# Kernel optimization log

Hardware: AMD Instinct MI355X
Metric: run time of the kernel (lower is better)

## Reference

```python
import jax, jax.numpy as jnp
import numpy as np

TEMP = 0.1
GROUPS = 16
EPS = 1e-5
COS_EPS = 1e-8


def _encoder(x, conv_w, conv_b, gn_g, gn_b):
    # Conv2d(C,C,3,pad=1) -> GroupNorm(16,C) -> ReLU -> AdaptiveAvgPool2d(1) -> Flatten
    y = jax.lax.conv_general_dilated(
        x, conv_w, window_strides=(1, 1), padding='SAME',
        dimension_numbers=('NCHW', 'OIHW', 'NCHW')) + conv_b[None, :, None, None]
    B, C, H, W = y.shape
    yg = y.reshape(B, GROUPS, C // GROUPS, H, W)
    mu = yg.mean(axis=(2, 3, 4), keepdims=True)
    var = yg.var(axis=(2, 3, 4), keepdims=True)
    yn = ((yg - mu) * jax.lax.rsqrt(var + EPS)).reshape(B, C, H, W)
    y = yn * gn_g[None, :, None, None] + gn_b[None, :, None, None]
    y = jax.nn.relu(y)
    return y.mean(axis=(2, 3))  # [B, C]


def _projector(h, w1, b1, w2, b2, ln_g, ln_b):
    h = jax.nn.relu(h @ w1 + b1)
    h = h @ w2 + b2
    mu = h.mean(axis=-1, keepdims=True)
    var = h.var(axis=-1, keepdims=True)
    return (h - mu) * jax.lax.rsqrt(var + EPS) * ln_g + ln_b


def _predictor(z, w1, b1, w2, b2):
    return jax.nn.relu(z @ w1 + b1) @ w2 + b2


def _l2norm(z):
    n = jnp.sqrt(jnp.sum(z * z, axis=1, keepdims=True))
    return z / jnp.maximum(n, COS_EPS)


def _pair_loss(zi, zj, off_idx):
    # vectorized version of the nested-loop cosine-sim + cross-entropy (label 0)
    S = (_l2norm(zi) @ _l2norm(zj).T) / TEMP  # [B, B]
    pos = jnp.diagonal(S)                     # sim(i_k, j_k)
    neg = jnp.take_along_axis(S, off_idx, axis=1)  # [B, B-1], row k = S[k, l!=k]
    logits = jnp.concatenate([pos[:, None], neg], axis=1)
    return jnp.mean(jax.nn.logsumexp(logits, axis=1) - logits[:, 0])


def setup_inputs() -> dict:
    key = jax.random.key(0)
    ks = jax.random.split(key, 32)
    B, C, H, W, P = 256, 256, 16, 16, 128
    d = {}
    d['x_t2w'] = jax.random.normal(ks[0], (B, C, H, W), jnp.float32)
    d['x_t2f'] = jax.random.normal(ks[1], (B, C, H, W), jnp.float32)
    d['x_t1n'] = jax.random.normal(ks[2], (B, C, H, W), jnp.float32)
    i = 3
    for m in ('t2w', 't2f', 't1n'):
        d[f'conv_w_{m}'] = jax.random.normal(ks[i], (C, C, 3, 3), jnp.float32) * 0.02; i += 1
        d[f'conv_b_{m}'] = jnp.zeros((C,), jnp.float32)
        d[f'gn_g_{m}'] = jnp.ones((C,), jnp.float32)
        d[f'gn_b_{m}'] = jnp.zeros((C,), jnp.float32)
    d['proj_w1'] = jax.random.normal(ks[i], (C, C), jnp.float32) * 0.02; i += 1
    d['proj_b1'] = jnp.zeros((C,), jnp.float32)
    d['proj_w2'] = jax.random.normal(ks[i], (C, P), jnp.float32) * 0.02; i += 1
    d['proj_b2'] = jnp.zeros((P,), jnp.float32)
    d['ln_g'] = jnp.ones((P,), jnp.float32)
    d['ln_b'] = jnp.zeros((P,), jnp.float32)
    d['pred_w1'] = jax.random.normal(ks[i], (P, P), jnp.float32) * 0.02; i += 1
    d['pred_b1'] = jnp.zeros((P,), jnp.float32)
    d['pred_w2'] = jax.random.normal(ks[i], (P, P), jnp.float32) * 0.02; i += 1
    d['pred_b2'] = jnp.zeros((P,), jnp.float32)
    return d


def reference(x_t2w, x_t2f, x_t1n,
              conv_w_t2w, conv_b_t2w, gn_g_t2w, gn_b_t2w,
              conv_w_t2f, conv_b_t2f, gn_g_t2f, gn_b_t2f,
              conv_w_t1n, conv_b_t1n, gn_g_t1n, gn_b_t1n,
              proj_w1, proj_b1, proj_w2, proj_b2, ln_g, ln_b,
              pred_w1, pred_b1, pred_w2, pred_b2):
    xs = [x_t2w, x_t2f, x_t1n]
    enc_params = [(conv_w_t2w, conv_b_t2w, gn_g_t2w, gn_b_t2w),
                  (conv_w_t2f, conv_b_t2f, gn_g_t2f, gn_b_t2f),
                  (conv_w_t1n, conv_b_t1n, gn_g_t1n, gn_b_t1n)]
    encoded = [_encoder(x, *p) for x, p in zip(xs, enc_params)]
    projected = [_projector(e, proj_w1, proj_b1, proj_w2, proj_b2, ln_g, ln_b) for e in encoded]
    preds = [_predictor(z, pred_w1, pred_b1, pred_w2, pred_b2) for z in projected]

    B = projected[0].shape[0]
    off_idx = jnp.asarray(np.array([[l for l in range(B) if l != k] for k in range(B)],
                                    dtype=np.int32))
    pairs = [(0, 1), (0, 2), (1, 2)]
    loss = sum(_pair_loss(projected[i], projected[j], off_idx) for i, j in pairs) / len(pairs)

    return (jnp.stack(encoded), jnp.stack(projected), jnp.stack(preds), loss)
```

## Files before the change

### kernel.cpp

```cpp
#include <hip/hip_runtime.h>
#include <hip/hip_bf16.h>

typedef float f32x4 __attribute__((ext_vector_type(4)));
typedef __bf16 bf16x8 __attribute__((ext_vector_type(8)));
typedef unsigned short u16x8 __attribute__((ext_vector_type(8)));

#define GN_EPS 1e-5f
#define LN_EPS 1e-5f
#define COS_EPS_F 1e-8f

__device__ __forceinline__ unsigned short f2bf(float f) {
  unsigned int u = __builtin_bit_cast(unsigned int, f);
  u += 0x7fffu + ((u >> 16) & 1u);
  return (unsigned short)(u >> 16);
}

__global__ void transpose_kernel(const float* __restrict__ x,
                                 unsigned short* __restrict__ xT) {
  __shared__ float lds[64][129];
  int bid = blockIdx.x;
  int hwt = bid & 3, cit = (bid >> 2) & 1, b = bid >> 3;
  int hw0 = hwt * 64, ci0 = cit * 128;
  int tid = threadIdx.x;

  int hwx = tid & 63, cy0 = tid >> 6;
  const float* xb = x + (b * 256 + ci0) * 256 + hw0;
  #pragma unroll 8
  for (int p = 0; p < 32; ++p) {
    int cy = cy0 + 4 * p;
    lds[hwx][cy] = xb[cy * 256 + hwx];
  }
  __syncthreads();

  int cp = tid & 63, hy0 = tid >> 6;
  unsigned int* outp = (unsigned int*)(xT + (b * 256 + hw0) * 256 + ci0);
  #pragma unroll 4
  for (int p = 0; p < 16; ++p) {
    int hy = hy0 + 4 * p;
    float lo = lds[hy][2 * cp];
    float hi = lds[hy][2 * cp + 1];
    unsigned int w = ((unsigned int)f2bf(hi) << 16) | f2bf(lo);
    outp[hy * 128 + cp] = w;
  }
}

__global__ void pack_kernel(const float* __restrict__ w, unsigned short* __restrict__ wp,
                            unsigned short* __restrict__ zerobuf) {
  int idx = blockIdx.x * 256 + threadIdx.x;
  if (blockIdx.x == 0 && threadIdx.x < 8) zerobuf[threadIdx.x] = 0;
  int ci = idx & 255;
  int rest = idx >> 8;
  int khw = rest % 9, co = rest / 9;
  wp[idx] = f2bf(w[(co * 256 + ci) * 9 + khw]);
}

__device__ __forceinline__ void gl_lds16(const unsigned short* g, unsigned short* l) {
  __builtin_amdgcn_global_load_lds(
      (const __attribute__((address_space(1))) void*)g,
      (__attribute__((address_space(3))) void*)l, 16, 0, 0);
}

__launch_bounds__(512, 2)
__global__ void conv_gn_pool(const unsigned short* __restrict__ xT,
                             const unsigned short* __restrict__ wp,
                             const unsigned short* __restrict__ zb,
                             const float* __restrict__ cbias,
                             const float* __restrict__ gng,
                             const float* __restrict__ gnb,
                             float* __restrict__ enc) {
  __shared__ unsigned short Ab[4][8192];
  __shared__ unsigned short Bb[4][8192];
  __shared__ float gsum[16], gsq[16], pooled[256];

  int bid = blockIdx.x;
  int b = (bid & 7) * 32 + (bid >> 3);
  int tid = threadIdx.x;
  int wid = tid >> 6, lane = tid & 63;
  int wr = wid >> 2, wc = wid & 3;
  int l15 = lane & 15, l4 = lane >> 4;

  if (tid < 16) { gsum[tid] = 0.f; gsq[tid] = 0.f; }
  if (tid < 256) pooled[tid] = 0.f;

  int s0 = tid, s1 = 512 + tid;
  int r0 = s0 >> 2, c0 = s0 & 3;
  int r1 = s1 >> 2, c1 = s1 & 3;
  int cs0 = (c0 ^ (r0 & 3)) * 8;
  int cs1 = (c1 ^ (r1 & 3)) * 8;
  int rh0 = r0 >> 4, rw0 = r0 & 15;
  int rh1 = r1 >> 4, rw1 = r1 & 15;

  const unsigned short* xb = xT + b * 65536;
  const unsigned short* bB0 = wp + r0 * 2304 + cs0;
  const unsigned short* bB1 = wp + r1 * 2304 + cs1;

  int kch = (l4 ^ (l15 & 3)) * 8;
  int base_af = (wr * 128 + l15) * 32 + kch;
  int base_bf = (wc * 64 + l15) * 32 + kch;

  f32x4 acc[8][4];
  #pragma unroll
  for (int i = 0; i < 8; ++i)
    #pragma unroll
    for (int j = 0; j < 4; ++j) acc[i][j] = (f32x4)(0.0f);

  #define STAGE_A(T2)                                                          \
    {                                                                          \
      int khw_ = (T2) >> 3, kc_ = (T2) & 7;                                    \
      int kh_ = khw_ / 3, kw_ = khw_ - kh_ * 3;                                \
      int ci0_ = kc_ * 32;                                                     \
      unsigned short* dst_ = &Ab[(T2) & 3][0];                                 \
      int h0_ = rh0 + kh_ - 1, w0_ = rw0 + kw_ - 1;                            \
      const unsigned short* sA0 = ((unsigned)h0_ < 16u && (unsigned)w0_ < 16u) \
          ? xb + ((h0_ * 16 + w0_) * 256 + ci0_ + cs0) : zb;                   \
      gl_lds16(sA0, dst_ + s0 * 8);                                            \
      int h1_ = rh1 + kh_ - 1, w1_ = rw1 + kw_ - 1;                            \
      const unsigned short* sA1 = ((unsigned)h1_ < 16u && (unsigned)w1_ < 16u) \
          ? xb + ((h1_ * 16 + w1_) * 256 + ci0_ + cs1) : zb;                   \
      gl_lds16(sA1, dst_ + s1 * 8);                                            \
    }
  #define STAGE_B(T2)                                                          \
    {                                                                          \
      int off_ = ((T2) >> 3) * 256 + ((T2) & 7) * 32;                          \
      unsigned short* dst_ = &Bb[(T2) & 3][0];                                 \
      gl_lds16(bB0 + off_, dst_ + s0 * 8);                                     \
      gl_lds16(bB1 + off_, dst_ + s1 * 8);                                     \
    }

  STAGE_A(0); STAGE_B(0); STAGE_A(1); STAGE_B(1);
  asm volatile("s_waitcnt vmcnt(4)" ::: "memory");
  __builtin_amdgcn_s_barrier();

  for (int t = 0; t < 72; ++t) {
    const unsigned short* Ap = &Ab[t & 3][0];
    const unsigned short* Bp = &Bb[t & 3][0];
    int tp2 = t + 2;
    bf16x8 af0[4], bfr[4];
    #pragma unroll
    for (int j = 0; j < 4; ++j)
      af0[j] = __builtin_bit_cast(bf16x8, *(const u16x8*)&Ap[base_af + j * 512]);
    #pragma unroll
    for (int n = 0; n < 4; ++n)
      bfr[n] = __builtin_bit_cast(bf16x8, *(const u16x8*)&Bp[base_bf + n * 512]);
    if (tp2 < 72) STAGE_A(tp2);
    __builtin_amdgcn_s_barrier();
    __builtin_amdgcn_s_setprio(1);
    #pragma unroll
    for (int j = 0; j < 4; ++j)
      #pragma unroll
      for (int n = 0; n < 4; ++n)
        acc[j][n] = __builtin_amdgcn_mfma_f32_16x16x32_bf16(af0[j], bfr[n], acc[j][n], 0, 0, 0);
    __builtin_amdgcn_s_setprio(0);
    __builtin_amdgcn_s_barrier();
    bf16x8 af1[4];
    #pragma unroll
    for (int j = 0; j < 4; ++j)
      af1[j] = __builtin_bit_cast(bf16x8, *(const u16x8*)&Ap[base_af + (4 + j) * 512]);
    if (tp2 < 72) STAGE_B(tp2);
    if (t < 69) asm volatile("s_waitcnt vmcnt(4)" ::: "memory");
    else        asm volatile("s_waitcnt vmcnt(0)" ::: "memory");
    __builtin_amdgcn_s_barrier();
    __builtin_amdgcn_s_setprio(1);
    #pragma unroll
    for (int j = 0; j < 4; ++j)
      #pragma unroll
      for (int n = 0; n < 4; ++n)
        acc[4 + j][n] = __builtin_amdgcn_mfma_f32_16x16x32_bf16(af1[j], bfr[n], acc[4 + j][n], 0, 0, 0);
    __builtin_amdgcn_s_setprio(0);
    __builtin_amdgcn_s_barrier();
  }
  #undef STAGE_A
  #undef STAGE_B

  float bias[4], ggv[4], gbv[4];
  #pragma unroll
  for (int nf = 0; nf < 4; ++nf) {
    int co = wc * 64 + nf * 16 + l15;
    bias[nf] = cbias[co]; ggv[nf] = gng[co]; gbv[nf] = gnb[co];
  }
  #pragma unroll
  for (int nf = 0; nf < 4; ++nf) {
    float s1 = 0.f, s2 = 0.f;
    #pragma unroll
    for (int mf = 0; mf < 8; ++mf)
      #pragma unroll
      for (int i = 0; i < 4; ++i) {
        float v = acc[mf][nf][i] + bias[nf];
        acc[mf][nf][i] = v;
        s1 += v; s2 += v * v;
      }
    #pragma unroll
    for (int d = 1; d < 64; d <<= 1) {
      s1 += __shfl_xor(s1, d);
      s2 += __shfl_xor(s2, d);
    }
    if (lane == 0) {
      atomicAdd(&gsum[wc * 4 + nf], s1);
      atomicAdd(&gsq[wc * 4 + nf], s2);
    }
  }
  __syncthreads();
  #pragma unroll
  for (int nf = 0; nf < 4; ++nf) {
    int g = wc * 4 + nf;
    float mean = gsum[g] * (1.f / 4096.f);
    float var = gsq[g] * (1.f / 4096.f) - mean * mean;
    float rs = rsqrtf(var + GN_EPS);
    float p = 0.f;
    #pragma unroll
    for (int mf = 0; mf < 8; ++mf)
      #pragma unroll
      for (int i = 0; i < 4; ++i) {
        float v = (acc[mf][nf][i] - mean) * rs * ggv[nf] + gbv[nf];
        p += fmaxf(v, 0.f);
      }
    p += __shfl_xor(p, 16);
    p += __shfl_xor(p, 32);
    if (lane < 16) atomicAdd(&pooled[wc * 64 + nf * 16 + l15], p);
  }
  __syncthreads();
  if (tid < 256)
    enc[b * 256 + tid] = pooled[tid] * (1.f / 256.f);
}

__global__ void proj_pred(const float* __restrict__ enc,
                          const float* __restrict__ w1, const float* __restrict__ b1,
                          const float* __restrict__ w2, const float* __restrict__ b2,
                          const float* __restrict__ lng, const float* __restrict__ lnb,
                          const float* __restrict__ pw1, const float* __restrict__ pb1,
                          const float* __restrict__ pw2, const float* __restrict__ pb2,
                          float* __restrict__ proj, float* __restrict__ pred,
                          float* __restrict__ znorm) {
  __shared__ float row[256], h1[256], zz[128], p1[128], red[2];
  int r = blockIdx.x, tid = threadIdx.x;
  row[tid] = enc[r * 256 + tid];
  __syncthreads();
  float a = 0.f;
  for (int k = 0; k < 256; ++k) a += row[k] * w1[k * 256 + tid];
  h1[tid] = fmaxf(a + b1[tid], 0.f);
  __syncthreads();
  if (tid < 128) {
    a = 0.f;
    for (int k = 0; k < 256; ++k) a += h1[k] * w2[k * 128 + tid];
    zz[tid] = a + b2[tid];
  }
  __syncthreads();
  if (tid == 0) {
    float m = 0.f;
    for (int k = 0; k < 128; ++k) m += zz[k];
    m *= (1.f / 128.f);
    float v = 0.f;
    for (int k = 0; k < 128; ++k) { float d = zz[k] - m; v += d * d; }
    red[0] = m;
    red[1] = rsqrtf(v * (1.f / 128.f) + LN_EPS);
  }
  __syncthreads();
  float zval = 0.f;
  if (tid < 128) {
    zval = (zz[tid] - red[0]) * red[1] * lng[tid] + lnb[tid];
    proj[r * 128 + tid] = zval;
  }
  __syncthreads();
  if (tid < 128) zz[tid] = zval;
  __syncthreads();
  if (tid == 0) {
    float s = 0.f;
    for (int k = 0; k < 128; ++k) s += zz[k] * zz[k];
    red[0] = 1.f / fmaxf(sqrtf(s), COS_EPS_F);
  }
  __syncthreads();
  if (tid < 128) {
    znorm[r * 128 + tid] = zz[tid] * red[0];
    a = 0.f;
    for (int k = 0; k < 128; ++k) a += zz[k] * pw1[k * 128 + tid];
    p1[tid] = fmaxf(a + pb1[tid], 0.f);
  }
  __syncthreads();
  if (tid < 128) {
    a = 0.f;
    for (int k = 0; k < 128; ++k) a += p1[k] * pw2[k * 128 + tid];
    pred[r * 128 + tid] = a + pb2[tid];
  }
}

__global__ void loss_kernel(const float* __restrict__ zn, float* __restrict__ part) {
  __shared__ float zi[128], sv[256], rbuf[256];
  int blk = blockIdx.x;
  int p = blk >> 8, k = blk & 255;
  int i = (p == 2) ? 1 : 0;
  int j = (p == 0) ? 1 : 2;
  int tid = threadIdx.x;
  if (tid < 128) zi[tid] = zn[(i * 256 + k) * 128 + tid];
  __syncthreads();
  const float4* zj = (const float4*)&zn[(j * 256 + tid) * 128];
  float s = 0.f;
  #pragma unroll 8
  for (int d = 0; d < 32; ++d) {
    float4 aq = *(const float4*)&zi[d * 4];
    float4 bq = zj[d];
    s += aq.x * bq.x + aq.y * bq.y + aq.z * bq.z + aq.w * bq.w;
  }
  s *= 10.0f;
  sv[tid] = s;
  rbuf[tid] = s;
  __syncthreads();
  for (int d = 128; d > 0; d >>= 1) {
    if (tid < d) rbuf[tid] = fmaxf(rbuf[tid], rbuf[tid + d]);
    __syncthreads();
  }
  float m = rbuf[0];
  __syncthreads();
  rbuf[tid] = expf(s - m);
  __syncthreads();
  for (int d = 128; d > 0; d >>= 1) {
    if (tid < d) rbuf[tid] += rbuf[tid + d];
    __syncthreads();
  }
  if (tid == 0) part[blk] = m + logf(rbuf[0]) - sv[k];
}

__global__ void finalize_loss(const float* __restrict__ part, float* __restrict__ out) {
  __shared__ float red[256];
  int tid = threadIdx.x;
  float s = 0.f;
  for (int idx = tid; idx < 768; idx += 256) s += part[idx];
  red[tid] = s;
  __syncthreads();
  for (int d = 128; d > 0; d >>= 1) {
    if (tid < d) red[tid] += red[tid + d];
    __syncthreads();
  }
  if (tid == 0) out[0] = red[0] * (1.f / 768.f);
}

extern "C" void kernel_launch(void* const* d_in, const int* in_sizes, int n_in,
                              void* d_out, int out_size, void* d_ws, size_t ws_size,
                              hipStream_t stream) {
  const float* x[3]  = {(const float*)d_in[0], (const float*)d_in[1], (const float*)d_in[2]};
  const float* cw[3] = {(const float*)d_in[3], (const float*)d_in[7], (const float*)d_in[11]};
  const float* cb[3] = {(const float*)d_in[4], (const float*)d_in[8], (const float*)d_in[12]};
  const float* gg[3] = {(const float*)d_in[5], (const float*)d_in[9], (const float*)d_in[13]};
  const float* gb[3] = {(const float*)d_in[6], (const float*)d_in[10], (const float*)d_in[14]};
  const float* p_w1 = (const float*)d_in[15];
  const float* p_b1 = (const float*)d_in[16];
  const float* p_w2 = (const float*)d_in[17];
  const float* p_b2 = (const float*)d_in[18];
  const float* ln_g = (const float*)d_in[19];
  const float* ln_b = (const float*)d_in[20];
  const float* q_w1 = (const float*)d_in[21];
  const float* q_b1 = (const float*)d_in[22];
  const float* q_w2 = (const float*)d_in[23];
  const float* q_b2 = (const float*)d_in[24];

  float* out = (float*)d_out;
  char* ws = (char*)d_ws;
  unsigned short* xT  = (unsigned short*)ws;
  unsigned short* wpk = (unsigned short*)(ws + 33554432);
  float* znorm = (float*)(ws + 34734080);
  float* part  = (float*)(ws + 35127296);
  unsigned short* zb = (unsigned short*)(ws + 35130368);

  float* enc  = out;
  float* proj = out + 196608;
  float* pred = out + 294912;
  float* lossp = out + 393216;

  for (int m = 0; m < 3; ++m) {
    transpose_kernel<<<dim3(2048), dim3(256), 0, stream>>>(x[m], xT);
    pack_kernel<<<dim3(2304), dim3(256), 0, stream>>>(cw[m], wpk, zb);
    conv_gn_pool<<<dim3(256), dim3(512), 0, stream>>>(xT, wpk, zb, cb[m], gg[m], gb[m],
                                                      enc + m * 65536);
  }
  proj_pred<<<dim3(768), dim3(256), 0, stream>>>(enc, p_w1, p_b1, p_w2, p_b2, ln_g, ln_b,
                                                 q_w1, q_b1, q_w2, q_b2, proj, pred, znorm);
  loss_kernel<<<dim3(768), dim3(256), 0, stream>>>(znorm, part);
  finalize_loss<<<dim3(1), dim3(256), 0, stream>>>(part, lossp);
}
```

Before: 335.6 us.

## Batch all three modalities into single transpose, pack and conv launches

Merges the per-modality transpose, weight-pack and conv+GroupNorm+pool launches into single launches covering all three modalities. This triples the conv grid to fill the GPU better (256 blocks only gave one block per CU) and cuts launch overhead. It also changes the LDS XOR swizzle to use row bits 1-2 instead of 0-1 to reduce bank conflicts. The merged path needs three times the xT workspace and falls back to per-modality launches if the workspace is too small.

```diff
diff --git a/kernel.cpp b/kernel.cpp
--- a/kernel.cpp
+++ b/kernel.cpp
@@ -15,10 +15,17 @@
   return (unsigned short)(u >> 16);
 }
 
-__global__ void transpose_kernel(const float* __restrict__ x,
-                                 unsigned short* __restrict__ xT) {
+__global__ void transpose_kernel(const float* __restrict__ x0,
+                                 const float* __restrict__ x1,
+                                 const float* __restrict__ x2,
+                                 unsigned short* __restrict__ xT,
+                                 unsigned int strideElems, int mBase) {
   __shared__ float lds[64][129];
-  int bid = blockIdx.x;
+  int m = mBase + (blockIdx.x >> 11);
+  int bid = blockIdx.x & 2047;
+  const float* x = (m == 0) ? x0 : ((m == 1) ? x1 : x2);
+  unsigned short* dst = xT + (unsigned int)(m - mBase) * strideElems;
+
   int hwt = bid & 3, cit = (bid >> 2) & 1, b = bid >> 3;
   int hw0 = hwt * 64, ci0 = cit * 128;
   int tid = threadIdx.x;
@@ -33,7 +40,7 @@
   __syncthreads();
 
   int cp = tid & 63, hy0 = tid >> 6;
-  unsigned int* outp = (unsigned int*)(xT + (b * 256 + hw0) * 256 + ci0);
+  unsigned int* outp = (unsigned int*)(dst + (b * 256 + hw0) * 256 + ci0);
   #pragma unroll 4
   for (int p = 0; p < 16; ++p) {
     int hy = hy0 + 4 * p;
@@ -44,14 +51,19 @@
   }
 }
 
-__global__ void pack_kernel(const float* __restrict__ w, unsigned short* __restrict__ wp,
+__global__ void pack_kernel(const float* __restrict__ w0,
+                            const float* __restrict__ w1,
+                            const float* __restrict__ w2,
+                            unsigned short* __restrict__ wp,
                             unsigned short* __restrict__ zerobuf) {
+  int m = blockIdx.y;
+  const float* w = (m == 0) ? w0 : ((m == 1) ? w1 : w2);
   int idx = blockIdx.x * 256 + threadIdx.x;
-  if (blockIdx.x == 0 && threadIdx.x < 8) zerobuf[threadIdx.x] = 0;
+  if (m == 0 && blockIdx.x == 0 && threadIdx.x < 8) zerobuf[threadIdx.x] = 0;
   int ci = idx & 255;
   int rest = idx >> 8;
   int khw = rest % 9, co = rest / 9;
-  wp[idx] = f2bf(w[(co * 256 + ci) * 9 + khw]);
+  wp[m * 589824 + idx] = f2bf(w[(co * 256 + ci) * 9 + khw]);
 }
 
 __device__ __forceinline__ void gl_lds16(const unsigned short* g, unsigned short* l) {
@@ -62,18 +74,27 @@
 
 __launch_bounds__(512, 2)
 __global__ void conv_gn_pool(const unsigned short* __restrict__ xT,
+                             unsigned int xTstride,
                              const unsigned short* __restrict__ wp,
                              const unsigned short* __restrict__ zb,
-                             const float* __restrict__ cbias,
-                             const float* __restrict__ gng,
-                             const float* __restrict__ gnb,
-                             float* __restrict__ enc) {
+                             const float* __restrict__ cb0, const float* __restrict__ cb1,
+                             const float* __restrict__ cb2,
+                             const float* __restrict__ gg0, const float* __restrict__ gg1,
+                             const float* __restrict__ gg2,
+                             const float* __restrict__ gb0, const float* __restrict__ gb1,
+                             const float* __restrict__ gb2,
+                             float* __restrict__ enc, int mBase) {
   __shared__ unsigned short Ab[4][8192];
   __shared__ unsigned short Bb[4][8192];
   __shared__ float gsum[16], gsq[16], pooled[256];
 
-  int bid = blockIdx.x;
-  int b = (bid & 7) * 32 + (bid >> 3);
+  int mm = mBase + (blockIdx.x >> 8);
+  int bb = blockIdx.x & 255;
+  int b = (bb & 7) * 32 + (bb >> 3);
+  const float* cbias = (mm == 0) ? cb0 : ((mm == 1) ? cb1 : cb2);
+  const float* gng   = (mm == 0) ? gg0 : ((mm == 1) ? gg1 : gg2);
+  const float* gnb   = (mm == 0) ? gb0 : ((mm == 1) ? gb1 : gb2);
+
   int tid = threadIdx.x;
   int wid = tid >> 6, lane = tid & 63;
   int wr = wid >> 2, wc = wid & 3;
@@ -85,16 +106,17 @@
   int s0 = tid, s1 = 512 + tid;
   int r0 = s0 >> 2, c0 = s0 & 3;
   int r1 = s1 >> 2, c1 = s1 & 3;
-  int cs0 = (c0 ^ (r0 & 3)) * 8;
-  int cs1 = (c1 ^ (r1 & 3)) * 8;
+  int cs0 = (c0 ^ ((r0 >> 1) & 3)) * 8;
+  int cs1 = (c1 ^ ((r1 >> 1) & 3)) * 8;
   int rh0 = r0 >> 4, rw0 = r0 & 15;
   int rh1 = r1 >> 4, rw1 = r1 & 15;
 
-  const unsigned short* xb = xT + b * 65536;
-  const unsigned short* bB0 = wp + r0 * 2304 + cs0;
-  const unsigned short* bB1 = wp + r1 * 2304 + cs1;
-
-  int kch = (l4 ^ (l15 & 3)) * 8;
+  const unsigned short* xb = xT + (unsigned int)(mm - mBase) * xTstride + b * 65536;
+  const unsigned short* wpm = wp + mm * 589824;
+  const unsigned short* bB0 = wpm + r0 * 2304 + cs0;
+  const unsigned short* bB1 = wpm + r1 * 2304 + cs1;
+
+  int kch = (l4 ^ ((l15 >> 1) & 3)) * 8;
   int base_af = (wr * 128 + l15) * 32 + kch;
   int base_bf = (wc * 64 + l15) * 32 + kch;
 
@@ -220,7 +242,7 @@
   }
   __syncthreads();
   if (tid < 256)
-    enc[b * 256 + tid] = pooled[tid] * (1.f / 256.f);
+    enc[mm * 65536 + b * 256 + tid] = pooled[tid] * (1.f / 256.f);
 }
 
 __global__ void proj_pred(const float* __restrict__ enc,
@@ -354,22 +376,36 @@
 
   float* out = (float*)d_out;
   char* ws = (char*)d_ws;
+
+  const size_t XT_ONE = 33554432;
+  bool merged = ws_size >= (3 * XT_ONE + 3538944 + 393216 + 3072 + 64);
+
+  size_t xt_total = merged ? 3 * XT_ONE : XT_ONE;
   unsigned short* xT  = (unsigned short*)ws;
-  unsigned short* wpk = (unsigned short*)(ws + 33554432);
-  float* znorm = (float*)(ws + 34734080);
-  float* part  = (float*)(ws + 35127296);
-  unsigned short* zb = (unsigned short*)(ws + 35130368);
+  unsigned short* wpk = (unsigned short*)(ws + xt_total);
+  float* znorm = (float*)(ws + xt_total + 3538944);
+  float* part  = (float*)(ws + xt_total + 3538944 + 393216);
+  unsigned short* zb = (unsigned short*)(ws + xt_total + 3538944 + 393216 + 3072);
 
   float* enc  = out;
   float* proj = out + 196608;
   float* pred = out + 294912;
   float* lossp = out + 393216;
 
-  for (int m = 0; m < 3; ++m) {
-    transpose_kernel<<<dim3(2048), dim3(256), 0, stream>>>(x[m], xT);
-    pack_kernel<<<dim3(2304), dim3(256), 0, stream>>>(cw[m], wpk, zb);
-    conv_gn_pool<<<dim3(256), dim3(512), 0, stream>>>(xT, wpk, zb, cb[m], gg[m], gb[m],
-                                                      enc + m * 65536);
+  pack_kernel<<<dim3(2304, 3), dim3(256), 0, stream>>>(cw[0], cw[1], cw[2], wpk, zb);
+
+  if (merged) {
+    transpose_kernel<<<dim3(6144), dim3(256), 0, stream>>>(x[0], x[1], x[2], xT, 16777216u, 0);
+    conv_gn_pool<<<dim3(768), dim3(512), 0, stream>>>(
+        xT, 16777216u, wpk, zb, cb[0], cb[1], cb[2], gg[0], gg[1], gg[2],
+        gb[0], gb[1], gb[2], enc, 0);
+  } else {
+    for (int m = 0; m < 3; ++m) {
+      transpose_kernel<<<dim3(2048), dim3(256), 0, stream>>>(x[0], x[1], x[2], xT, 0u, m);
+      conv_gn_pool<<<dim3(256), dim3(512), 0, stream>>>(
+          xT, 0u, wpk, zb, cb[0], cb[1], cb[2], gg[0], gg[1], gg[2],
+          gb[0], gb[1], gb[2], enc, m);
+    }
   }
   proj_pred<<<dim3(768), dim3(256), 0, stream>>>(enc, p_w1, p_b1, p_w2, p_b2, ln_g, ln_b,
                                                  q_w1, q_b1, q_w2, q_b2, proj, pred, znorm);
```

Measured after the change: 318.4 us. -5.1%, faster.
